# Kernel optimization log

Measured on AMD Instinct MI355X. Metric: run time of the kernel, lower is better.

Reference implementation:

```python
import jax, jax.numpy as jnp
import numpy as np

B, F, T, K = 131072, 1024, 100, 32  # batch, num_features, num_trees, features per tree (sqrt(F))


def setup_inputs() -> dict:
    key = jax.random.key(0)
    kx, kw = jax.random.split(key)
    x = jax.random.normal(kx, (B, F), dtype=jnp.float32)
    # per-tree random feature selection without replacement (np.random.choice replace=False)
    rng = np.random.default_rng(0)
    idx = np.argsort(rng.random((T, F)), axis=1)[:, :K].astype(np.int32)
    feature_indices = jnp.asarray(idx)
    feature_thresholds = jnp.zeros((T, K), dtype=jnp.float32)  # lazy-init zeros in original
    feature_weights = jax.random.uniform(kw, (T, K), dtype=jnp.float32)  # torch.rand
    return {
        "x": x,
        "feature_indices": feature_indices,
        "feature_thresholds": feature_thresholds,
        "feature_weights": feature_weights,
    }


def reference(x, feature_indices, feature_thresholds, feature_weights):
    # Per tree t: ws_t = sum_k (x[:, idx[t,k]] - thr[t,k]) * w[t,k]
    # Equivalent fused form: scatter weights into a dense [T, F] matrix and do one GEMM,
    # with per-tree bias sum_k thr*w. scatter-add handles any duplicate indices identically
    # to the gather-then-sum formulation.
    T_, K_ = feature_indices.shape
    tree_ids = jnp.arange(T_, dtype=feature_indices.dtype)[:, None]  # [T,1]
    W_full = jnp.zeros((T_, x.shape[1]), dtype=x.dtype).at[tree_ids, feature_indices].add(feature_weights)
    bias = jnp.sum(feature_thresholds * feature_weights, axis=1)  # [T]
    ws = x @ W_full.T - bias[None, :]  # [B, T]
    p = jax.nn.sigmoid(ws)
    pm = jnp.mean(p, axis=1)  # mean over trees; mean(1-p) = 1 - mean(p)
    return jnp.stack([1.0 - pm, pm], axis=1)  # [B, 2]
```

## Files before the change

### kernel.cpp

```cpp
#include <hip/hip_runtime.h>
#include <math.h>

constexpr int Bn = 131072;
constexpr int Fn = 1024;
constexpr int Tn = 100;
constexpr int Kn = 32;

constexpr int TP  = 112;
constexpr int NF  = TP / 16;
constexpr int BK  = 64;
constexpr int NT  = Fn / BK;
constexpr int BM  = 128;
constexpr int MW  = 32;
constexpr int WPB = 4;
constexpr int BLOCK = 256;
constexpr int GRID  = Bn / BM;

typedef __attribute__((ext_vector_type(8))) short bf16x8;
typedef __attribute__((ext_vector_type(4))) float f32x4;

__device__ inline unsigned short f2bf(float f) {
    uint32_t u = __float_as_uint(f);
    return (unsigned short)((u + 0x7FFFu + ((u >> 16) & 1u)) >> 16);
}

__device__ inline bf16x8 cvt8(f32x4 lo, f32x4 hi) {
    bf16x8 v;
    v[0] = (short)f2bf(lo[0]); v[1] = (short)f2bf(lo[1]);
    v[2] = (short)f2bf(lo[2]); v[3] = (short)f2bf(lo[3]);
    v[4] = (short)f2bf(hi[0]); v[5] = (short)f2bf(hi[1]);
    v[6] = (short)f2bf(hi[2]); v[7] = (short)f2bf(hi[3]);
    return v;
}

__global__ __launch_bounds__(64)
void rf_prep(const int* __restrict__ fidx, const float* __restrict__ fthr,
             const float* __restrict__ fw,
             unsigned short* __restrict__ wt, float* __restrict__ bias)
{
    const int t    = blockIdx.x;
    const int lane = threadIdx.x;

    int4 z = make_int4(0, 0, 0, 0);
    int4* rowp = (int4*)(wt + (size_t)t * Fn);
    rowp[lane * 2 + 0] = z;
    rowp[lane * 2 + 1] = z;
    __syncthreads();

    float bsum = 0.f;
    if (t < Tn && lane < Kn) {
        const int   idx = fidx[t * Kn + lane];
        const float w   = fw[t * Kn + lane];
        const float th  = fthr[t * Kn + lane];
        wt[(size_t)t * Fn + idx] = f2bf(w);
        bsum = th * w;
    }
#pragma unroll
    for (int d = 1; d < 64; d <<= 1) bsum += __shfl_xor(bsum, d, 64);
    if (lane == 0) bias[t] = (t < Tn) ? bsum : 0.f;
}


#define NTLD8(T, S) do {                                                   \
    const char* _p = paA + (size_t)(T) * 256;                              \
    S##0 = __builtin_nontemporal_load((const f32x4*)(_p + 0 * 16384));     \
    S##1 = __builtin_nontemporal_load((const f32x4*)(_p + 1 * 16384));     \
    S##2 = __builtin_nontemporal_load((const f32x4*)(_p + 2 * 16384));     \
    S##3 = __builtin_nontemporal_load((const f32x4*)(_p + 3 * 16384));     \
    S##4 = __builtin_nontemporal_load((const f32x4*)(_p + 4 * 16384));     \
    S##5 = __builtin_nontemporal_load((const f32x4*)(_p + 5 * 16384));     \
    S##6 = __builtin_nontemporal_load((const f32x4*)(_p + 6 * 16384));     \
    S##7 = __builtin_nontemporal_load((const f32x4*)(_p + 7 * 16384));     \
} while (0)

#define DSWR8(BUFB, S) do {                                                \
    *(f32x4*)(lbase + (BUFB) + w0) = S##0;                                 \
    *(f32x4*)(lbase + (BUFB) + w1) = S##1;                                 \
    *(f32x4*)(lbase + (BUFB) + w2) = S##2;                                 \
    *(f32x4*)(lbase + (BUFB) + w3) = S##3;                                 \
    *(f32x4*)(lbase + (BUFB) + w4) = S##4;                                 \
    *(f32x4*)(lbase + (BUFB) + w5) = S##5;                                 \
    *(f32x4*)(lbase + (BUFB) + w6) = S##6;                                 \
    *(f32x4*)(lbase + (BUFB) + w7) = S##7;                                 \
} while (0)

#define LOADB(T) do {                                                      \
    const char* _q = pbB + (size_t)(T) * 128;                              \
    B00 = *(const bf16x8*)(_q + 0 * 32768);                                \
    B01 = *(const bf16x8*)(_q + 1 * 32768);                                \
    B02 = *(const bf16x8*)(_q + 2 * 32768);                                \
    B03 = *(const bf16x8*)(_q + 3 * 32768);                                \
    B04 = *(const bf16x8*)(_q + 4 * 32768);                                \
    B05 = *(const bf16x8*)(_q + 5 * 32768);                                \
    B06 = *(const bf16x8*)(_q + 6 * 32768);                                \
    B10 = *(const bf16x8*)(_q + 0 * 32768 + 64);                           \
    B11 = *(const bf16x8*)(_q + 1 * 32768 + 64);                           \
    B12 = *(const bf16x8*)(_q + 2 * 32768 + 64);                           \
    B13 = *(const bf16x8*)(_q + 3 * 32768 + 64);                           \
    B14 = *(const bf16x8*)(_q + 4 * 32768 + 64);                           \
    B15 = *(const bf16x8*)(_q + 5 * 32768 + 64);                           \
    B16 = *(const bf16x8*)(_q + 6 * 32768 + 64);                           \
} while (0)

#define READF(M, KS, LO, HI, BUFB) do {                                    \
    const char* _b = lbase + (BUFB) + ((M) * 16 + r) * 256;                \
    LO = *(const f32x4*)(_b + ((((KS) * 8 + g2 + 0) ^ r) * 16));           \
    HI = *(const f32x4*)(_b + ((((KS) * 8 + g2 + 1) ^ r) * 16));           \
} while (0)

#define MFMAROW(AF, Ba,Bb,Bc,Bd,Be,Bf,Bg, a0,a1,a2,a3,a4,a5,a6) do {       \
    a0 = __builtin_amdgcn_mfma_f32_16x16x32_bf16(AF, Ba, a0, 0, 0, 0);     \
    a1 = __builtin_amdgcn_mfma_f32_16x16x32_bf16(AF, Bb, a1, 0, 0, 0);     \
    a2 = __builtin_amdgcn_mfma_f32_16x16x32_bf16(AF, Bc, a2, 0, 0, 0);     \
    a3 = __builtin_amdgcn_mfma_f32_16x16x32_bf16(AF, Bd, a3, 0, 0, 0);     \
    a4 = __builtin_amdgcn_mfma_f32_16x16x32_bf16(AF, Be, a4, 0, 0, 0);     \
    a5 = __builtin_amdgcn_mfma_f32_16x16x32_bf16(AF, Bf, a5, 0, 0, 0);     \
    a6 = __builtin_amdgcn_mfma_f32_16x16x32_bf16(AF, Bg, a6, 0, 0, 0);     \
} while (0)

#define PHASE(TC, CB, OB, W, I) do {                                       \
    if ((TC) + 2 < NT) NTLD8((TC) + 2, I);                                 \
    LOADB(TC);                                                             \
    READF(0, 0, L0, L1, CB);                                               \
    READF(1, 0, L2, L3, CB);                                               \
    READF(0, 1, L4, L5, CB);                                               \
    READF(1, 1, L6, L7, CB);                                               \
    asm volatile("s_waitcnt vmcnt(22)" ::: "memory");   \
    if ((TC) + 1 < NT) DSWR8(OB, W);                                       \
    __builtin_amdgcn_s_setprio(1);                                         \
    {                                                                      \
        bf16x8 _af;                                                        \
        _af = cvt8(L0, L1);                                                \
        MFMAROW(_af, B00, B01, B02, B03, B04, B05, B06,                    \
                acc00, acc01, acc02, acc03, acc04, acc05, acc06);          \
        _af = cvt8(L2, L3);                                                \
        MFMAROW(_af, B00, B01, B02, B03, B04, B05, B06,                    \
                acc10, acc11, acc12, acc13, acc14, acc15, acc16);          \
        _af = cvt8(L4, L5);                                                \
        MFMAROW(_af, B10, B11, B12, B13, B14, B15, B16,                    \
                acc00, acc01, acc02, acc03, acc04, acc05, acc06);          \
        _af = cvt8(L6, L7);                                                \
        MFMAROW(_af, B10, B11, B12, B13, B14, B15, B16,                    \
                acc10, acc11, acc12, acc13, acc14, acc15, acc16);          \
    }                                                                      \
    __builtin_amdgcn_s_setprio(0);                                         \
} while (0)

__global__ __launch_bounds__(BLOCK)
void rf_gemm(const float* __restrict__ x,
             const unsigned short* __restrict__ wt,
             const float* __restrict__ bias,
             float* __restrict__ out)
{
    __shared__ float lds[WPB][2][MW * BK];

    const int lane = threadIdx.x & 63;
    const int wid  = threadIdx.x >> 6;
    const int rb   = blockIdx.x * BM;
    const int r    = lane & 15;
    const int g    = lane >> 4;
    const int g2   = g * 2;
    const int sub  = lane >> 4;
    const int c    = lane & 15;

    const char* paA = (const char*)(x + (size_t)(rb + wid * MW + sub) * Fn) + c * 16;
    const char* pbB = (const char*)(wt + (size_t)r * Fn + g * 8);
    char* lbase = (char*)&lds[wid][0][0];

    const int w0 = (0 * 4 + sub) * 256 + ((c ^ ((0 * 4 + sub) & 15)) * 16);
    const int w1 = (1 * 4 + sub) * 256 + ((c ^ ((1 * 4 + sub) & 15)) * 16);
    const int w2 = (2 * 4 + sub) * 256 + ((c ^ ((2 * 4 + sub) & 15)) * 16);
    const int w3 = (3 * 4 + sub) * 256 + ((c ^ ((3 * 4 + sub) & 15)) * 16);
    const int w4 = (4 * 4 + sub) * 256 + ((c ^ ((4 * 4 + sub) & 15)) * 16);
    const int w5 = (5 * 4 + sub) * 256 + ((c ^ ((5 * 4 + sub) & 15)) * 16);
    const int w6 = (6 * 4 + sub) * 256 + ((c ^ ((6 * 4 + sub) & 15)) * 16);
    const int w7 = (7 * 4 + sub) * 256 + ((c ^ ((7 * 4 + sub) & 15)) * 16);

    f32x4 acc00 = {0,0,0,0}, acc01 = {0,0,0,0}, acc02 = {0,0,0,0},
          acc03 = {0,0,0,0}, acc04 = {0,0,0,0}, acc05 = {0,0,0,0},
          acc06 = {0,0,0,0};
    f32x4 acc10 = {0,0,0,0}, acc11 = {0,0,0,0}, acc12 = {0,0,0,0},
          acc13 = {0,0,0,0}, acc14 = {0,0,0,0}, acc15 = {0,0,0,0},
          acc16 = {0,0,0,0};

    f32x4 SA0, SA1, SA2, SA3, SA4, SA5, SA6, SA7;
    f32x4 SB0, SB1, SB2, SB3, SB4, SB5, SB6, SB7;
    f32x4 L0, L1, L2, L3, L4, L5, L6, L7;
    bf16x8 B00, B01, B02, B03, B04, B05, B06;
    bf16x8 B10, B11, B12, B13, B14, B15, B16;

    NTLD8(0, SA);
    DSWR8(0, SA);
    NTLD8(1, SB);

    for (int t = 0; t < NT; t += 2) {
        PHASE(t,     0,    8192, SB, SA);
        PHASE(t + 1, 8192, 0,    SA, SB);
    }

    f32x4 accA[2][NF] = {
        { acc00, acc01, acc02, acc03, acc04, acc05, acc06 },
        { acc10, acc11, acc12, acc13, acc14, acc15, acc16 }
    };

    const int col = lane & 15;
    float psum[2][4] = {};
#pragma unroll
    for (int f = 0; f < NF; ++f) {
        const int  n     = f * 16 + col;
        const bool valid = n < Tn;
        const float bv   = bias[n];
#pragma unroll
        for (int m = 0; m < 2; ++m)
#pragma unroll
            for (int q = 0; q < 4; ++q) {
                const float ws = accA[m][f][q] - bv;
                const float p  = 1.f / (1.f + __expf(-ws));
                if (valid) psum[m][q] += p;
            }
    }
#pragma unroll
    for (int m = 0; m < 2; ++m)
#pragma unroll
        for (int q = 0; q < 4; ++q)
#pragma unroll
            for (int d = 1; d < 16; d <<= 1)
                psum[m][q] += __shfl_xor(psum[m][q], d, 64);

#pragma unroll
    for (int m = 0; m < 2; ++m) {
        if (col < 4) {
            const int q   = col;
            const int row = rb + wid * MW + m * 16 + g * 4 + q;
            const float pm = psum[m][q] * (1.0f / Tn);
            *(float2*)(out + (size_t)row * 2) = make_float2(1.0f - pm, pm);
        }
    }
}

extern "C" void kernel_launch(void* const* d_in, const int* in_sizes, int n_in,
                              void* d_out, int out_size, void* d_ws, size_t ws_size,
                              hipStream_t stream) {
    const float* x    = (const float*)d_in[0];
    const int*   fidx = (const int*)  d_in[1];
    const float* fthr = (const float*)d_in[2];
    const float* fw   = (const float*)d_in[3];
    float*       out  = (float*)d_out;

    unsigned short* wt   = (unsigned short*)d_ws;
    float*          bias = (float*)((char*)d_ws + (size_t)TP * Fn * 2);

    rf_prep<<<TP, 64, 0, stream>>>(fidx, fthr, fw, wt, bias);
    rf_gemm<<<GRID, BLOCK, 0, stream>>>(x, wt, bias, out);
}
```

Before: 166.8 us.

## Halve per-wave row tile to 16 rows and raise occupancy via launch bounds

Measured after the change: 234.8 us. 1.41x slower.

```diff
diff --git a/kernel.cpp b/kernel.cpp
--- a/kernel.cpp
+++ b/kernel.cpp
@@ -10,9 +10,9 @@
 constexpr int NF  = TP / 16;
 constexpr int BK  = 64;
 constexpr int NT  = Fn / BK;
-constexpr int BM  = 128;
-constexpr int MW  = 32;
+constexpr int MW  = 16;
 constexpr int WPB = 4;
+constexpr int BM  = WPB * MW;
 constexpr int BLOCK = 256;
 constexpr int GRID  = Bn / BM;
 
@@ -61,27 +61,19 @@
 }
 
 
-#define NTLD8(T, S) do {                                                   \
+#define NTLD4(T, S) do {                                                   \
     const char* _p = paA + (size_t)(T) * 256;                              \
     S##0 = __builtin_nontemporal_load((const f32x4*)(_p + 0 * 16384));     \
     S##1 = __builtin_nontemporal_load((const f32x4*)(_p + 1 * 16384));     \
     S##2 = __builtin_nontemporal_load((const f32x4*)(_p + 2 * 16384));     \
     S##3 = __builtin_nontemporal_load((const f32x4*)(_p + 3 * 16384));     \
-    S##4 = __builtin_nontemporal_load((const f32x4*)(_p + 4 * 16384));     \
-    S##5 = __builtin_nontemporal_load((const f32x4*)(_p + 5 * 16384));     \
-    S##6 = __builtin_nontemporal_load((const f32x4*)(_p + 6 * 16384));     \
-    S##7 = __builtin_nontemporal_load((const f32x4*)(_p + 7 * 16384));     \
-} while (0)
-
-#define DSWR8(BUFB, S) do {                                                \
+} while (0)
+
+#define DSWR4(BUFB, S) do {                                                \
     *(f32x4*)(lbase + (BUFB) + w0) = S##0;                                 \
     *(f32x4*)(lbase + (BUFB) + w1) = S##1;                                 \
     *(f32x4*)(lbase + (BUFB) + w2) = S##2;                                 \
     *(f32x4*)(lbase + (BUFB) + w3) = S##3;                                 \
-    *(f32x4*)(lbase + (BUFB) + w4) = S##4;                                 \
-    *(f32x4*)(lbase + (BUFB) + w5) = S##5;                                 \
-    *(f32x4*)(lbase + (BUFB) + w6) = S##6;                                 \
-    *(f32x4*)(lbase + (BUFB) + w7) = S##7;                                 \
 } while (0)
 
 #define LOADB(T) do {                                                      \
@@ -102,51 +94,41 @@
     B16 = *(const bf16x8*)(_q + 6 * 32768 + 64);                           \
 } while (0)
 
-#define READF(M, KS, LO, HI, BUFB) do {                                    \
-    const char* _b = lbase + (BUFB) + ((M) * 16 + r) * 256;                \
+#define READF(KS, LO, HI, BUFB) do {                                       \
+    const char* _b = lbase + (BUFB) + r * 256;                             \
     LO = *(const f32x4*)(_b + ((((KS) * 8 + g2 + 0) ^ r) * 16));           \
     HI = *(const f32x4*)(_b + ((((KS) * 8 + g2 + 1) ^ r) * 16));           \
 } while (0)
 
-#define MFMAROW(AF, Ba,Bb,Bc,Bd,Be,Bf,Bg, a0,a1,a2,a3,a4,a5,a6) do {       \
-    a0 = __builtin_amdgcn_mfma_f32_16x16x32_bf16(AF, Ba, a0, 0, 0, 0);     \
-    a1 = __builtin_amdgcn_mfma_f32_16x16x32_bf16(AF, Bb, a1, 0, 0, 0);     \
-    a2 = __builtin_amdgcn_mfma_f32_16x16x32_bf16(AF, Bc, a2, 0, 0, 0);     \
-    a3 = __builtin_amdgcn_mfma_f32_16x16x32_bf16(AF, Bd, a3, 0, 0, 0);     \
-    a4 = __builtin_amdgcn_mfma_f32_16x16x32_bf16(AF, Be, a4, 0, 0, 0);     \
-    a5 = __builtin_amdgcn_mfma_f32_16x16x32_bf16(AF, Bf, a5, 0, 0, 0);     \
-    a6 = __builtin_amdgcn_mfma_f32_16x16x32_bf16(AF, Bg, a6, 0, 0, 0);     \
+#define MFMAROW(AF, Ba,Bb,Bc,Bd,Be,Bf,Bg) do {                             \
+    acc0 = __builtin_amdgcn_mfma_f32_16x16x32_bf16(AF, Ba, acc0, 0, 0, 0); \
+    acc1 = __builtin_amdgcn_mfma_f32_16x16x32_bf16(AF, Bb, acc1, 0, 0, 0); \
+    acc2 = __builtin_amdgcn_mfma_f32_16x16x32_bf16(AF, Bc, acc2, 0, 0, 0); \
+    acc3 = __builtin_amdgcn_mfma_f32_16x16x32_bf16(AF, Bd, acc3, 0, 0, 0); \
+    acc4 = __builtin_amdgcn_mfma_f32_16x16x32_bf16(AF, Be, acc4, 0, 0, 0); \
+    acc5 = __builtin_amdgcn_mfma_f32_16x16x32_bf16(AF, Bf, acc5, 0, 0, 0); \
+    acc6 = __builtin_amdgcn_mfma_f32_16x16x32_bf16(AF, Bg, acc6, 0, 0, 0); \
 } while (0)
 
 #define PHASE(TC, CB, OB, W, I) do {                                       \
-    if ((TC) + 2 < NT) NTLD8((TC) + 2, I);                                 \
     LOADB(TC);                                                             \
-    READF(0, 0, L0, L1, CB);                                               \
-    READF(1, 0, L2, L3, CB);                                               \
-    READF(0, 1, L4, L5, CB);                                               \
-    READF(1, 1, L6, L7, CB);                                               \
-    asm volatile("s_waitcnt vmcnt(22)" ::: "memory");   \
-    if ((TC) + 1 < NT) DSWR8(OB, W);                                       \
-    __builtin_amdgcn_s_setprio(1);                                         \
+    READF(0, L0, L1, CB);                                                  \
+    READF(1, L2, L3, CB);                                                  \
+    if ((TC) + 1 < NT) {                                                   \
+        asm volatile("s_waitcnt vmcnt(14)" ::: "memory");  \
+        DSWR4(OB, W);                                                      \
+    }                                                                      \
+    if ((TC) + 2 < NT) NTLD4((TC) + 2, I);                                 \
     {                                                                      \
         bf16x8 _af;                                                        \
         _af = cvt8(L0, L1);                                                \
-        MFMAROW(_af, B00, B01, B02, B03, B04, B05, B06,                    \
-                acc00, acc01, acc02, acc03, acc04, acc05, acc06);          \
+        MFMAROW(_af, B00, B01, B02, B03, B04, B05, B06);                   \
         _af = cvt8(L2, L3);                                                \
-        MFMAROW(_af, B00, B01, B02, B03, B04, B05, B06,                    \
-                acc10, acc11, acc12, acc13, acc14, acc15, acc16);          \
-        _af = cvt8(L4, L5);                                                \
-        MFMAROW(_af, B10, B11, B12, B13, B14, B15, B16,                    \
-                acc00, acc01, acc02, acc03, acc04, acc05, acc06);          \
-        _af = cvt8(L6, L7);                                                \
-        MFMAROW(_af, B10, B11, B12, B13, B14, B15, B16,                    \
-                acc10, acc11, acc12, acc13, acc14, acc15, acc16);          \
+        MFMAROW(_af, B10, B11, B12, B13, B14, B15, B16);                   \
     }                                                                      \
-    __builtin_amdgcn_s_setprio(0);                                         \
-} while (0)
-
-__global__ __launch_bounds__(BLOCK)
+} while (0)
+
+__global__ __launch_bounds__(BLOCK, 3)
 void rf_gemm(const float* __restrict__ x,
              const unsigned short* __restrict__ wt,
              const float* __restrict__ bias,
@@ -171,70 +153,53 @@
     const int w1 = (1 * 4 + sub) * 256 + ((c ^ ((1 * 4 + sub) & 15)) * 16);
     const int w2 = (2 * 4 + sub) * 256 + ((c ^ ((2 * 4 + sub) & 15)) * 16);
     const int w3 = (3 * 4 + sub) * 256 + ((c ^ ((3 * 4 + sub) & 15)) * 16);
-    const int w4 = (4 * 4 + sub) * 256 + ((c ^ ((4 * 4 + sub) & 15)) * 16);
-    const int w5 = (5 * 4 + sub) * 256 + ((c ^ ((5 * 4 + sub) & 15)) * 16);
-    const int w6 = (6 * 4 + sub) * 256 + ((c ^ ((6 * 4 + sub) & 15)) * 16);
-    const int w7 = (7 * 4 + sub) * 256 + ((c ^ ((7 * 4 + sub) & 15)) * 16);
-
-    f32x4 acc00 = {0,0,0,0}, acc01 = {0,0,0,0}, acc02 = {0,0,0,0},
-          acc03 = {0,0,0,0}, acc04 = {0,0,0,0}, acc05 = {0,0,0,0},
-          acc06 = {0,0,0,0};
-    f32x4 acc10 = {0,0,0,0}, acc11 = {0,0,0,0}, acc12 = {0,0,0,0},
-          acc13 = {0,0,0,0}, acc14 = {0,0,0,0}, acc15 = {0,0,0,0},
-          acc16 = {0,0,0,0};
-
-    f32x4 SA0, SA1, SA2, SA3, SA4, SA5, SA6, SA7;
-    f32x4 SB0, SB1, SB2, SB3, SB4, SB5, SB6, SB7;
-    f32x4 L0, L1, L2, L3, L4, L5, L6, L7;
+
+    f32x4 acc0 = {0,0,0,0}, acc1 = {0,0,0,0}, acc2 = {0,0,0,0},
+          acc3 = {0,0,0,0}, acc4 = {0,0,0,0}, acc5 = {0,0,0,0},
+          acc6 = {0,0,0,0};
+
+    f32x4 SA0, SA1, SA2, SA3;
+    f32x4 SB0, SB1, SB2, SB3;
+    f32x4 L0, L1, L2, L3;
     bf16x8 B00, B01, B02, B03, B04, B05, B06;
     bf16x8 B10, B11, B12, B13, B14, B15, B16;
 
-    NTLD8(0, SA);
-    DSWR8(0, SA);
-    NTLD8(1, SB);
+    NTLD4(0, SA);
+    DSWR4(0, SA);
+    NTLD4(1, SB);
 
     for (int t = 0; t < NT; t += 2) {
-        PHASE(t,     0,    8192, SB, SA);
-        PHASE(t + 1, 8192, 0,    SA, SB);
-    }
-
-    f32x4 accA[2][NF] = {
-        { acc00, acc01, acc02, acc03, acc04, acc05, acc06 },
-        { acc10, acc11, acc12, acc13, acc14, acc15, acc16 }
-    };
+        PHASE(t,     0,    4096, SB, SA);
+        PHASE(t + 1, 4096, 0,    SA, SB);
+    }
+
+    f32x4 accA[NF] = { acc0, acc1, acc2, acc3, acc4, acc5, acc6 };
 
     const int col = lane & 15;
-    float psum[2][4] = {};
+    float psum[4] = {};
 #pragma unroll
     for (int f = 0; f < NF; ++f) {
         const int  n     = f * 16 + col;
         const bool valid = n < Tn;
         const float bv   = bias[n];
 #pragma unroll
-        for (int m = 0; m < 2; ++m)
-#pragma unroll
-            for (int q = 0; q < 4; ++q) {
-                const float ws = accA[m][f][q] - bv;
-                const float p  = 1.f / (1.f + __expf(-ws));
-                if (valid) psum[m][q] += p;
-            }
-    }
-#pragma unroll
-    for (int m = 0; m < 2; ++m)
-#pragma unroll
-        for (int q = 0; q < 4; ++q)
-#pragma unroll
-            for (int d = 1; d < 16; d <<= 1)
-                psum[m][q] += __shfl_xor(psum[m][q], d, 64);
-
-#pragma unroll
-    for (int m = 0; m < 2; ++m) {
-        if (col < 4) {
-            const int q   = col;
-            const int row = rb + wid * MW + m * 16 + g * 4 + q;
-            const float pm = psum[m][q] * (1.0f / Tn);
-            *(float2*)(out + (size_t)row * 2) = make_float2(1.0f - pm, pm);
+        for (int q = 0; q < 4; ++q) {
+            const float ws = accA[f][q] - bv;
+            const float p  = 1.f / (1.f + __expf(-ws));
+            if (valid) psum[q] += p;
         }
+    }
+#pragma unroll
+    for (int q = 0; q < 4; ++q)
+#pragma unroll
+        for (int d = 1; d < 16; d <<= 1)
+            psum[q] += __shfl_xor(psum[q], d, 64);
+
+    if (col < 4) {
+        const int q   = col;
+        const int row = rb + wid * MW + g * 4 + q;
+        const float pm = psum[q] * (1.0f / Tn);
+        *(float2*)(out + (size_t)row * 2) = make_float2(1.0f - pm, pm);
     }
 }
 
```
